# Optimization experiments

Measured on AMD Instinct MI355X. Metric: run time of the kernel, lower is better.

The kernel has to match this reference:

```python
import jax, jax.numpy as jnp
import numpy as np

N = 4
SEGMENTS = 16
IN_F = 256
OUT_F = 256
BATCH = 512


def chebyshev_lobatto(n):
    # Chebyshev-Lobatto interpolation nodes on [-1, 1]
    k = jnp.arange(n, dtype=jnp.float32)
    return -jnp.cos(jnp.pi * k / (n - 1))


def lagrange_basis(x, nodes):
    # x: [B, In]; returns basis values [B, In, n]
    n = nodes.shape[0]
    cols = []
    for j in range(n):  # n is a small static constant (4)
        terms = [(x - nodes[m]) / (nodes[j] - nodes[m]) for m in range(n) if m != j]
        cols.append(jnp.prod(jnp.stack(terms, axis=0), axis=0))
    return jnp.stack(cols, axis=-1)


def setup_inputs() -> dict:
    key = jax.random.key(0)
    k1, k2 = jax.random.split(key)
    x = jax.random.uniform(k1, (BATCH, IN_F), dtype=jnp.float32, minval=-1.0, maxval=1.0)
    w = jax.random.uniform(
        k2, (OUT_F, IN_F, (N - 1) * SEGMENTS + 1), dtype=jnp.float32, minval=-1.0, maxval=1.0
    )
    return {"x": x, "w": w, "n": N, "segments": SEGMENTS}


def reference(x, w, n, segments):
    nodes = chebyshev_lobatto(n)
    # segment id per element, clamped to [0, segments-1]
    id_min = jnp.clip(((x + 1.0) / 2.0 * segments).astype(jnp.int32), 0, segments - 1)
    id_max = id_min + 1
    wid_min = id_min * (n - 1)  # start of weight slice; slice length == n
    # segment boundaries in x-space: eta(i) = i/segments * 2 - 1
    x_min = id_min.astype(x.dtype) / segments * 2.0 - 1.0
    x_max = id_max.astype(x.dtype) / segments * 2.0 - 1.0
    # rescale x into [-1, 1] within its segment
    x_in = 2.0 * (x - x_min) / (x_max - x_min) - 1.0
    basis = lagrange_basis(x_in, nodes)  # [B, In, n]
    # gather per-element weight slice: w_g[b,i,j,o] = w[o, i, wid_min[b,i]+j]
    idx = wid_min[..., None] + jnp.arange(n)  # [B, In, n]
    w_t = jnp.transpose(w, (1, 2, 0))  # [In, K, Out]
    in_f = w.shape[1]
    w_g = w_t[jnp.arange(in_f)[None, :, None], idx]  # [B, In, n, Out]
    # interpolate and sum over in_features (matches einsum 'ijk,jkli->jl')
    return jnp.einsum("bin,bino->bo", basis, w_g)
```

## Files before the change

kernel.cpp:

```cpp
#include <hip/hip_runtime.h>


#define INF     256
#define OUTF    256
#define WSTRIDE 49
#define OSTRIDE (INF * WSTRIDE)

#define NSPLIT  32
#define IPB     8
#define ICH     2

#define GLOAD_LDS(gptr, lptr)                                                       \
  __builtin_amdgcn_global_load_lds(                                                 \
      (const __attribute__((address_space(1))) unsigned int*)(gptr),                \
      (__attribute__((address_space(3))) unsigned int*)(lptr), 4, 0, 0)

#define STAGE(ci)                                                                   \
do {                                                                                \
    float* lbase_ = &smem[((ci) & 1) * 8192];                                       \
    _Pragma("unroll")                                                               \
    for (int t = 0; t < 32; ++t) {                                                  \
        int r_ = t * 4 + wave;                              \
        int i_loc_ = r_ >> 6, o_ = r_ & 63;                                         \
        const float* gp_ = w + (size_t)(o_base + o_) * OSTRIDE                      \
                             + (i_base + (ci) * ICH + i_loc_) * WSTRIDE + lane_t;   \
        GLOAD_LDS(gp_, lbase_ + r_ * 64);                                           \
    }                                                                               \
} while (0)

#define COMPUTE(ci)                                                                 \
do {                                                                                \
    _Pragma("unroll")                                                               \
    for (int il = 0; il < ICH; ++il) {                                              \
        const int ig_ = (ci) * ICH + il;                                            \
        const float* p_ = &smem[((ci) & 1) * 8192 +                                 \
                                (il * 64 + oh * 32) * 64 + sseg[ig_] * 4];          \
        const float c0_ = c[ig_][0], c1_ = c[ig_][1];                               \
        const float c2_ = c[ig_][2], c3_ = c[ig_][3];                               \
        _Pragma("unroll")                                                           \
        for (int oo = 0; oo < 32; ++oo) {                                           \
            float4 wv_ = *(const float4*)(p_ + oo * 64);                            \
            acc[oo] += c0_ * wv_.x + c1_ * wv_.y + c2_ * wv_.z + c3_ * wv_.w;       \
        }                                                                           \
    }                                                                               \
} while (0)

__global__ __launch_bounds__(256, 2)
void pp_partial(const float* __restrict__ x, const float* __restrict__ w,
                float* __restrict__ ws) {
    __shared__ float smem[16384];

    const int tid  = threadIdx.x;
    const int wave = tid >> 6, lane = tid & 63;
    const int isplit = blockIdx.x;
    const int i_base = isplit * IPB;
    const int o_base = blockIdx.y * 64;
    const int b_base = blockIdx.z * 128;
    const int bh = wave >> 1, oh = wave & 1;
    const int b  = b_base + bh * 64 + lane;
    const int lane_t = 3 * (lane >> 2) + (lane & 3);

    float c[IPB][4];
    int   sseg[IPB];
    {
        const float4* xp = (const float4*)(x + (size_t)b * INF + i_base);
        float4 x0 = xp[0], x1 = xp[1];
        float xs[8] = {x0.x, x0.y, x0.z, x0.w, x1.x, x1.y, x1.z, x1.w};
        #pragma unroll
        for (int i = 0; i < IPB; ++i) {
            float xx = xs[i];
            int id = (int)((xx + 1.0f) * 8.0f);
            id = id < 0 ? 0 : (id > 15 ? 15 : id);
            float u = (xx - ((float)id * 0.125f - 1.0f)) * 16.0f - 1.0f;
            float a = u + 1.0f, b2 = u + 0.5f, cc = u - 0.5f, d = u - 1.0f;
            c[i][0] = b2 * cc * d  * (-2.0f / 3.0f);
            c[i][1] = a  * cc * d  * ( 4.0f / 3.0f);
            c[i][2] = a  * b2 * d  * (-4.0f / 3.0f);
            c[i][3] = a  * b2 * cc * ( 2.0f / 3.0f);
            sseg[i] = id;
        }
    }

    float acc[32];
    #pragma unroll
    for (int q = 0; q < 32; ++q) acc[q] = 0.0f;

    STAGE(0);
    __syncthreads();
    STAGE(1); COMPUTE(0); __syncthreads();
    STAGE(2); COMPUTE(1); __syncthreads();
    STAGE(3); COMPUTE(2); __syncthreads();
    COMPUTE(3);

    float4* wp = (float4*)(ws + (size_t)isplit * (512 * 256)
                              + (size_t)b * 256 + o_base + oh * 32);
    #pragma unroll
    for (int q = 0; q < 8; ++q)
        wp[q] = make_float4(acc[4*q], acc[4*q+1], acc[4*q+2], acc[4*q+3]);
}

__global__ __launch_bounds__(256)
void pp_reduce(const float* __restrict__ ws, float* __restrict__ out) {
    const size_t off = (size_t)blockIdx.x * 256 + threadIdx.x;
    float s = 0.0f;
    #pragma unroll
    for (int k = 0; k < NSPLIT; ++k)
        s += ws[(size_t)k * (512 * 256) + off];
    out[off] = s;
}

extern "C" void kernel_launch(void* const* d_in, const int* in_sizes, int n_in,
                              void* d_out, int out_size, void* d_ws, size_t ws_size,
                              hipStream_t stream) {
    const float* x = (const float*)d_in[0];
    const float* w = (const float*)d_in[1];
    float* out = (float*)d_out;
    float* ws  = (float*)d_ws;
    (void)ws_size; (void)n_in; (void)in_sizes; (void)out_size;

    dim3 grid(NSPLIT, 4, 4);
    pp_partial<<<grid, 256, 0, stream>>>(x, w, ws);
    pp_reduce<<<dim3(512), 256, 0, stream>>>(ws, out);
}
```

Measured before the change: 87.87 us.

## Pre-expand weights to fp16 segment-packed layout and use fdot2 accumulation

Adds a pre-pass that converts the weight tensor into fp16 pairs, expanded per segment (16 segments x 4 coefficients) and laid out contiguously per (in, out). The partial kernel then stages this packed buffer with 16-byte global-to-LDS loads and computes the interpolation with packed fp16 dot products, with smaller batch tiles and higher occupancy. The aim is to halve the bytes moved and the LDS traffic. The cost is an extra kernel pass over all weights each call and lower precision for weights and coefficients (round-toward-zero fp16), which may break accuracy tolerance.

```diff
diff --git a/kernel.cpp b/kernel.cpp
--- a/kernel.cpp
+++ b/kernel.cpp
@@ -1,67 +1,92 @@
 #include <hip/hip_runtime.h>
 
+
+typedef _Float16 h2 __attribute__((ext_vector_type(2)));
 
 #define INF     256
 #define OUTF    256
 #define WSTRIDE 49
 #define OSTRIDE (INF * WSTRIDE)
-
 #define NSPLIT  32
 #define IPB     8
-#define ICH     2
+#define WE_UINTS (256 * 256 * 32)
 
-#define GLOAD_LDS(gptr, lptr)                                                       \
+#define GLOAD16(gptr, lptr)                                                         \
   __builtin_amdgcn_global_load_lds(                                                 \
       (const __attribute__((address_space(1))) unsigned int*)(gptr),                \
-      (__attribute__((address_space(3))) unsigned int*)(lptr), 4, 0, 0)
+      (__attribute__((address_space(3))) unsigned int*)(lptr), 16, 0, 0)
+
+__global__ __launch_bounds__(256)
+void pp_expand(const float* __restrict__ w, unsigned int* __restrict__ we) {
+    const int i = blockIdx.x;
+    const int o = threadIdx.x;
+    const float* src = w + (size_t)o * OSTRIDE + i * WSTRIDE;
+    float t[49];
+    #pragma unroll
+    for (int k = 0; k < 49; ++k) t[k] = src[k];
+    unsigned int pk[32];
+    #pragma unroll
+    for (int s = 0; s < 16; ++s) {
+        auto p0 = __builtin_amdgcn_cvt_pkrtz(t[3*s],   t[3*s+1]);
+        auto p1 = __builtin_amdgcn_cvt_pkrtz(t[3*s+2], t[3*s+3]);
+        pk[2*s]   = __builtin_bit_cast(unsigned int, p0);
+        pk[2*s+1] = __builtin_bit_cast(unsigned int, p1);
+    }
+    uint4* dst = (uint4*)(we + ((size_t)i * 256 + o) * 32);
+    #pragma unroll
+    for (int k = 0; k < 8; ++k)
+        dst[k] = make_uint4(pk[4*k], pk[4*k+1], pk[4*k+2], pk[4*k+3]);
+}
 
 #define STAGE(ci)                                                                   \
 do {                                                                                \
-    float* lbase_ = &smem[((ci) & 1) * 8192];                                       \
+    unsigned int* lds_ = &smem[((ci) & 1) * 4096];                                  \
     _Pragma("unroll")                                                               \
-    for (int t = 0; t < 32; ++t) {                                                  \
-        int r_ = t * 4 + wave;                              \
-        int i_loc_ = r_ >> 6, o_ = r_ & 63;                                         \
-        const float* gp_ = w + (size_t)(o_base + o_) * OSTRIDE                      \
-                             + (i_base + (ci) * ICH + i_loc_) * WSTRIDE + lane_t;   \
-        GLOAD_LDS(gp_, lbase_ + r_ * 64);                                           \
+    for (int it = 0; it < 4; ++it) {                                                \
+        int f_ = it * 256 + tid;                            \
+        int iloc_ = f_ >> 9;                                                        \
+        int rem_  = f_ & 511;                                                       \
+        const unsigned int* gp_ = we + ((size_t)(i_base + (ci)*2 + iloc_) * 256     \
+                                        + o_base) * 32 + rem_ * 4;                  \
+        GLOAD16(gp_, lds_ + f_ * 4);                                                \
     }                                                                               \
 } while (0)
 
 #define COMPUTE(ci)                                                                 \
 do {                                                                                \
     _Pragma("unroll")                                                               \
-    for (int il = 0; il < ICH; ++il) {                                              \
-        const int ig_ = (ci) * ICH + il;                                            \
-        const float* p_ = &smem[((ci) & 1) * 8192 +                                 \
-                                (il * 64 + oh * 32) * 64 + sseg[ig_] * 4];          \
-        const float c0_ = c[ig_][0], c1_ = c[ig_][1];                               \
-        const float c2_ = c[ig_][2], c3_ = c[ig_][3];                               \
+    for (int il = 0; il < 2; ++il) {                                                \
+        const int ig_ = (ci) * 2 + il;                                              \
+        const unsigned int* p_ = &smem[((ci) & 1) * 4096                            \
+                                       + (il * 64 + o_off) * 32 + sseg[ig_] * 2];   \
+        const h2 cA_ = ch01[ig_], cB_ = ch23[ig_];                                  \
         _Pragma("unroll")                                                           \
-        for (int oo = 0; oo < 32; ++oo) {                                           \
-            float4 wv_ = *(const float4*)(p_ + oo * 64);                            \
-            acc[oo] += c0_ * wv_.x + c1_ * wv_.y + c2_ * wv_.z + c3_ * wv_.w;       \
+        for (int oo = 0; oo < 16; ++oo) {                                           \
+            uint2 v_ = *(const uint2*)(p_ + oo * 32);                               \
+            acc[oo] = __builtin_amdgcn_fdot2(__builtin_bit_cast(h2, v_.x), cA_,     \
+                                             acc[oo], false);                       \
+            acc[oo] = __builtin_amdgcn_fdot2(__builtin_bit_cast(h2, v_.y), cB_,     \
+                                             acc[oo], false);                       \
         }                                                                           \
     }                                                                               \
 } while (0)
 
-__global__ __launch_bounds__(256, 2)
-void pp_partial(const float* __restrict__ x, const float* __restrict__ w,
-                float* __restrict__ ws) {
-    __shared__ float smem[16384];
+__global__ __launch_bounds__(256, 4)
+void pp_partial(const float* __restrict__ x, const unsigned int* __restrict__ we,
+                float* __restrict__ part) {
+    __shared__ unsigned int smem[8192];
 
     const int tid  = threadIdx.x;
     const int wave = tid >> 6, lane = tid & 63;
     const int isplit = blockIdx.x;
     const int i_base = isplit * IPB;
     const int o_base = blockIdx.y * 64;
-    const int b_base = blockIdx.z * 128;
-    const int bh = wave >> 1, oh = wave & 1;
-    const int b  = b_base + bh * 64 + lane;
-    const int lane_t = 3 * (lane >> 2) + (lane & 3);
+    const int b_base = blockIdx.z * 64;
+    const int b = b_base + lane;
+    const int o_off = wave * 16;
 
-    float c[IPB][4];
-    int   sseg[IPB];
+    int sseg[IPB];
+    h2  ch01[IPB], ch23[IPB];
     {
         const float4* xp = (const float4*)(x + (size_t)b * INF + i_base);
         float4 x0 = xp[0], x1 = xp[1];
@@ -73,17 +98,20 @@
             id = id < 0 ? 0 : (id > 15 ? 15 : id);
             float u = (xx - ((float)id * 0.125f - 1.0f)) * 16.0f - 1.0f;
             float a = u + 1.0f, b2 = u + 0.5f, cc = u - 0.5f, d = u - 1.0f;
-            c[i][0] = b2 * cc * d  * (-2.0f / 3.0f);
-            c[i][1] = a  * cc * d  * ( 4.0f / 3.0f);
-            c[i][2] = a  * b2 * d  * (-4.0f / 3.0f);
-            c[i][3] = a  * b2 * cc * ( 2.0f / 3.0f);
+            float c0 = b2 * cc * d  * (-2.0f / 3.0f);
+            float c1 = a  * cc * d  * ( 4.0f / 3.0f);
+            float c2 = a  * b2 * d  * (-4.0f / 3.0f);
+            float c3 = a  * b2 * cc * ( 2.0f / 3.0f);
+            h2 pA; pA[0] = (_Float16)c0; pA[1] = (_Float16)c1;
+            h2 pB; pB[0] = (_Float16)c2; pB[1] = (_Float16)c3;
+            ch01[i] = pA; ch23[i] = pB;
             sseg[i] = id;
         }
     }
 
-    float acc[32];
+    float acc[16];
     #pragma unroll
-    for (int q = 0; q < 32; ++q) acc[q] = 0.0f;
+    for (int q = 0; q < 16; ++q) acc[q] = 0.0f;
 
     STAGE(0);
     __syncthreads();
@@ -92,20 +120,20 @@
     STAGE(3); COMPUTE(2); __syncthreads();
     COMPUTE(3);
 
-    float4* wp = (float4*)(ws + (size_t)isplit * (512 * 256)
-                              + (size_t)b * 256 + o_base + oh * 32);
+    float4* wp = (float4*)(part + (size_t)isplit * (512 * 256)
+                                + (size_t)b * 256 + o_base + o_off);
     #pragma unroll
-    for (int q = 0; q < 8; ++q)
+    for (int q = 0; q < 4; ++q)
         wp[q] = make_float4(acc[4*q], acc[4*q+1], acc[4*q+2], acc[4*q+3]);
 }
 
 __global__ __launch_bounds__(256)
-void pp_reduce(const float* __restrict__ ws, float* __restrict__ out) {
+void pp_reduce(const float* __restrict__ part, float* __restrict__ out) {
     const size_t off = (size_t)blockIdx.x * 256 + threadIdx.x;
     float s = 0.0f;
     #pragma unroll
     for (int k = 0; k < NSPLIT; ++k)
-        s += ws[(size_t)k * (512 * 256) + off];
+        s += part[(size_t)k * (512 * 256) + off];
     out[off] = s;
 }
 
@@ -115,10 +143,11 @@
     const float* x = (const float*)d_in[0];
     const float* w = (const float*)d_in[1];
     float* out = (float*)d_out;
-    float* ws  = (float*)d_ws;
+    unsigned int* we = (unsigned int*)d_ws;
+    float* part = (float*)((char*)d_ws + (size_t)WE_UINTS * 4);
     (void)ws_size; (void)n_in; (void)in_sizes; (void)out_size;
 
-    dim3 grid(NSPLIT, 4, 4);
-    pp_partial<<<grid, 256, 0, stream>>>(x, w, ws);
-    pp_reduce<<<dim3(512), 256, 0, stream>>>(ws, out);
+    pp_expand<<<dim3(256), 256, 0, stream>>>(w, we);
+    pp_partial<<<dim3(NSPLIT, 4, 8), 256, 0, stream>>>(x, we, part);
+    pp_reduce<<<dim3(512), 256, 0, stream>>>(part, out);
 }
```

Result: slower. 91.75 us (+4.4%).
